# Kernel optimization log

Measured on AMD Instinct MI355X. Metric: run time of the kernel, lower is better.

## Reference

```python
import jax, jax.numpy as jnp
import numpy as np

N, E, M, NT, RB, SH, NIR, LAT = 10000, 160000, 8, 4, 8, 9, 3, 128
AVG_N = 16.0
LATF = LAT + M * NIR  # 152
COMP2IR = np.array([0, 1, 1, 1, 2, 2, 2, 2, 2])  # irrep id per SH component (0e,1o,2e)
IR1H = jnp.asarray(np.eye(NIR, dtype=np.float32)[COMP2IR])  # [9,3] one-hot comp->irrep


def _silu(x):
    return x * jax.nn.sigmoid(x)


def setup_inputs() -> dict:
    key = jax.random.key(0)
    ks = jax.random.split(key, 16)
    def w(k, shape, fan_in):
        return jax.random.normal(k, shape, jnp.float32) / np.sqrt(fan_in)
    return {
        'edge_attrs': jax.random.normal(ks[0], (E, SH), jnp.float32),
        'edge_embedding': jax.random.normal(ks[1], (E, RB), jnp.float32),
        'node_attrs': jax.random.uniform(ks[2], (N, NT), jnp.float32),
        'edge_lengths': jax.random.uniform(ks[3], (E,), jnp.float32),
        'tb_w0': w(ks[4], (2 * NT + RB, LAT), 2 * NT + RB),
        'tb_w1': w(ks[5], (LAT, LAT), LAT),
        'tb_w2': w(ks[6], (LAT, LAT), LAT),
        'env_mlp_w0': w(ks[7], (LAT, 2 * M * NIR), LAT),
        'env_mlp_w1': w(ks[8], (LAT, M * NIR), LAT),
        'env_linear_w': w(ks[9], (2, NIR, M, M), M),
        'latent_w': w(ks[10], (LATF, LAT), LATF),
        'lat2feat_w': w(ks[11], (2, LATF, NIR * M * M), LATF),
        'lat2featold_w': w(ks[12], (2, LATF, NIR * M * M), LATF),
        'final_w': w(ks[13], (LATF, M), LATF),
        'edge_index': jax.random.randint(ks[14], (2, E), 0, N, jnp.int32),
    }


def reference(edge_attrs, edge_embedding, node_attrs, edge_lengths,
              tb_w0, tb_w1, tb_w2, env_mlp_w0, env_mlp_w1, env_linear_w,
              latent_w, lat2feat_w, lat2featold_w, final_w, edge_index):
    center, neigh = edge_index[0], edge_index[1]
    n_nodes = node_attrs.shape[0]
    c2i = jnp.asarray(COMP2IR)

    # polynomial cutoff, p=6, x = r / r_max
    x = edge_lengths
    p = 6.0
    cut = (1.0 - (p + 1) * (p + 2) / 2 * x**6 + p * (p + 2) * x**7 - p * (p + 1) / 2 * x**8)
    cut = jnp.where(x < 1.0, cut, 0.0)[:, None]

    # two-body latent MLP on [center species, neighbor species, radial basis]
    tb_in = jnp.concatenate([node_attrs[center], node_attrs[neigh], edge_embedding], axis=-1)
    h = _silu(tb_in @ tb_w0)
    h = _silu(h @ tb_w1)
    latents = (h @ tb_w2) * cut  # [E, LAT]

    def weight_edges(wch):  # MakeWeightedChannels: per-irrep channel weights
        return wch[:, :, c2i] * edge_attrs[:, None, :]  # [E, M, 9]

    def env_of(w_cur, layer):  # scatter to node env + env linear
        env = jax.ops.segment_sum(weight_edges(w_cur), center, num_segments=n_nodes) / AVG_N
        Wc = env_linear_w[layer][c2i]  # [9, M, M]
        return jnp.einsum('duv,nvd->nud', Wc, env) / np.sqrt(M)

    def interact(features, env_c):  # scalar-gated equivariant coupling
        return features * env_c[:, :, :1] + env_c * features[:, :, :1]

    def invariants(f):  # per-(channel, irrep) norms
        return jnp.sqrt(jnp.einsum('eud,di->eui', f * f, IR1H) + 1e-8).reshape(f.shape[0], M * NIR)

    def pe_linear(Wflat, f):  # per-edge generated irrep-wise Linear
        W = Wflat.reshape(-1, NIR, M, M)
        return jnp.einsum('eiuv,di,evd->eud', W, IR1H, f) / np.sqrt(M)

    # ---- layer 0 (initial weighter + env weighter) ----
    ew = latents @ env_mlp_w0  # [E, 2*M*NIR]
    w_init = ew[:, :M * NIR].reshape(-1, M, NIR)
    w_cur = ew[:, M * NIR:].reshape(-1, M, NIR)
    features = weight_edges(w_init)  # [E, M, 9]
    env_c = env_of(w_cur, 0)[center]
    new_f = interact(features, env_c)
    lat_full = jnp.concatenate([latents, invariants(new_f)], axis=-1)  # [E, 152]
    features = 0.5 * pe_linear(lat_full @ lat2featold_w[0], features) \
             + 0.5 * pe_linear(lat_full @ lat2feat_w[0], new_f)

    # ---- layer 1 ----
    lat_new = _silu(lat_full @ latent_w) * cut
    latents = 0.5 * latents + 0.5 * lat_new  # latent resnet, sigmoid(0)=0.5
    w_cur = (latents @ env_mlp_w1).reshape(-1, M, NIR)
    env_c = env_of(w_cur, 1)[center]
    new_f = interact(features, env_c)
    lat_full = jnp.concatenate([latents, invariants(new_f)], axis=-1)
    features = 0.5 * pe_linear(lat_full @ lat2featold_w[1], features) \
             + 0.5 * pe_linear(lat_full @ lat2feat_w[1], new_f)

    # ---- final: generated linear to 1x1o per edge (components 1:4) ----
    wfin = lat_full @ final_w  # [E, M]
    return jnp.einsum('em,emd->ed', wfin, features[:, :, 1:4]) / np.sqrt(M)
```

## Files before the change

### kernel.cpp

```cpp
#include <hip/hip_runtime.h>
#include <hip/hip_bf16.h>

#define EE 160000
#define NNODES 10000

using bf16 = __hip_bfloat16;
using bf16x8 = __attribute__((ext_vector_type(8))) short;
using short4v = __attribute__((ext_vector_type(4))) short;
using f32x4  = __attribute__((ext_vector_type(4))) float;

__device__ __forceinline__ float silu_f(float x) { return x / (1.0f + __expf(-x)); }
__device__ __forceinline__ float b2f(bf16 v) { return __bfloat162float(v); }
__device__ __forceinline__ bf16 f2b(float v) { return __float2bfloat16(v); }

__device__ __forceinline__ unsigned bfbits(float v) {
    union { float f; unsigned u; } a; a.f = v;
    return (a.u + 0x7fffu + ((a.u >> 16) & 1u)) >> 16;
}
__device__ __forceinline__ unsigned pack2(float a, float b) {
    return bfbits(a) | (bfbits(b) << 16);
}
__device__ __forceinline__ void unpack2(unsigned u, float& a, float& b) {
    union { unsigned x; float f; } lo, hi;
    lo.x = u << 16; hi.x = u & 0xffff0000u;
    a = lo.f; b = hi.f;
}
__device__ __forceinline__ float bs2f(short s) {
    union { unsigned u; float f; } x; x.u = ((unsigned)(unsigned short)s) << 16;
    return x.f;
}

#define INV_AVGN_SQM 0.02209708691207961f
#define HALF_INV_SQM 0.17677669529663687f
#define INV_SQM      0.35355339059327373f

__global__ void kCnt(const int* __restrict__ eidx, int* __restrict__ deg)
{
    const int e = blockIdx.x * 256 + threadIdx.x;
    atomicAdd(&deg[eidx[e]], 1);
}

__global__ void kScan(const int* __restrict__ deg, int* __restrict__ off)
{
    __shared__ int part[256];
    const int t = threadIdx.x;
    int loc[40];
    int s = 0;
#pragma unroll
    for (int i = 0; i < 40; i++) {
        const int idx = t * 40 + i;
        const int v = (idx < NNODES) ? deg[idx] : 0;
        loc[i] = s;
        s += v;
    }
    part[t] = s;
    __syncthreads();
    for (int d = 1; d < 256; d <<= 1) {
        const int v = (t >= d) ? part[t - d] : 0;
        __syncthreads();
        part[t] += v;
        __syncthreads();
    }
    const int base = (t == 0) ? 0 : part[t - 1];
#pragma unroll
    for (int i = 0; i < 40; i++) {
        const int idx = t * 40 + i;
        if (idx < NNODES) off[idx] = base + loc[i];
    }
    if (t == 255) off[NNODES] = part[255];
}

__global__ void kFill(const int* __restrict__ eidx, int* __restrict__ cur,
                      const int* __restrict__ off, int* __restrict__ elist)
{
    const int e = blockIdx.x * 256 + threadIdx.x;
    const int c = eidx[e];
    const int pos = atomicAdd(&cur[c], 1);
    elist[off[c] + pos] = e;
}

__global__ void kPrepA(const float* __restrict__ w1, const float* __restrict__ w2,
                       const float* __restrict__ wm0, short* __restrict__ wAtF)
{
    const int t = blockIdx.x * 256 + threadIdx.x;
    if (t >= 38912) return;
    const int k = t & 127, c = t >> 7;
    float v;
    if (c < 128)      v = w1[k * 128 + c];
    else if (c < 256) v = w2[k * 128 + (c - 128)];
    else              v = wm0[k * 48 + (c - 256)];
    wAtF[((k >> 3) * 304 + c) * 8 + (k & 7)] = (short)bfbits(v);
}

__global__ void kPrepB(const float* __restrict__ l2fo, const float* __restrict__ l2fn,
                       const float* __restrict__ latw, const float* __restrict__ l2fo1,
                       const float* __restrict__ l2fn1, const float* __restrict__ finw,
                       const float* __restrict__ wm1, short* __restrict__ BtF)
{
    const int k = blockIdx.y;
    const int col = blockIdx.x * 256 + threadIdx.x;
    if (col >= 672) return;
    float v = 0.f;
    if (col < 648) {
        if (k < 152) {
            if (col < 384) {
                const int ir = col >> 7, half = (col >> 6) & 1, q = col & 63;
                const float* src = half ? l2fn : l2fo;
                v = src[k * 192 + ir * 64 + q];
            } else if (col < 512)  v = latw[k * 128 + (col - 384)];
            else if (col < 576)    v = l2fo1[k * 192 + 64 + (col - 512)];
            else if (col < 640)    v = l2fn1[k * 192 + 64 + (col - 576)];
            else                   v = finw[k * 8 + (col - 640)];
        }
    } else {
        if (k < 128) v = wm1[k * 24 + (col - 648)];
    }
    BtF[((k >> 3) * 672 + col) * 8 + (k & 7)] = (short)bfbits(v);
}

__global__ void kEnvG(const float* __restrict__ wcur, const float* __restrict__ ea,
                      const int* __restrict__ off, const int* __restrict__ elist,
                      const float* __restrict__ wl, float* __restrict__ envc)
{
    const int t = blockIdx.x * 256 + threadIdx.x;
    if (t >= NNODES * 9) return;
    const int n = t / 9;
    const int d = t - n * 9;
    const int irr = (d == 0) ? 0 : ((d < 4) ? 1 : 2);
    float v[8];
#pragma unroll
    for (int q = 0; q < 8; q++) v[q] = 0.0f;
    const int b = off[n], en = off[n + 1];
    for (int j = b; j < en; j++) {
        const int e = elist[j];
        const float ad = ea[e * 9 + d];
        const float* wr = wcur + (size_t)e * 24 + irr;
#pragma unroll
        for (int q = 0; q < 8; q++) v[q] = fmaf(wr[q * 3], ad, v[q]);
    }
#pragma unroll
    for (int u = 0; u < 8; u++) {
        float s = 0.0f;
#pragma unroll
        for (int q = 0; q < 8; q++) s = fmaf(wl[irr * 64 + u * 8 + q], v[q], s);
        envc[n * 72 + u * 9 + d] = s * INV_AVGN_SQM;
    }
}

__global__ __launch_bounds__(256) void kA0(
    const float* __restrict__ ea, const float* __restrict__ eemb,
    const float* __restrict__ nat, const float* __restrict__ elen,
    const float* __restrict__ w0, const int* __restrict__ eidx,
    short* __restrict__ h08, short* __restrict__ latf8s,
    bf16* __restrict__ eaT, float* __restrict__ cutb)
{
    __shared__ float w0s[16 * 128];
    const int t = threadIdx.x;
    const int e = blockIdx.x * 256 + t;
#pragma unroll
    for (int p = 0; p < 8; p++) { const int idx = p * 256 + t; w0s[idx] = w0[idx]; }
    __syncthreads();

    const int ctr = eidx[e];
    const int ngb = eidx[EE + e];
    float tin[16];
#pragma unroll
    for (int k = 0; k < 4; k++) tin[k] = nat[ctr * 4 + k];
#pragma unroll
    for (int k = 0; k < 4; k++) tin[4 + k] = nat[ngb * 4 + k];
#pragma unroll
    for (int k = 0; k < 8; k++) tin[8 + k] = eemb[e * 8 + k];

    const float x = elen[e];
    const float x2 = x * x, x4 = x2 * x2, x6 = x4 * x2, x7 = x6 * x, x8 = x7 * x;
    float cutv = 1.0f - 28.0f * x6 + 48.0f * x7 - 21.0f * x8;
    cutv = (x < 1.0f) ? cutv : 0.0f;
    cutb[e] = cutv;

    const size_t tb = (size_t)(e >> 5);
    const int el = e & 31;
#pragma unroll
    for (int jc = 0; jc < 4; jc++) {
        float a[32];
#pragma unroll
        for (int j = 0; j < 32; j++) a[j] = 0.0f;
#pragma unroll
        for (int k = 0; k < 16; k++) {
            const float v = tin[k];
#pragma unroll
            for (int j = 0; j < 32; j++) a[j] = fmaf(v, w0s[k * 128 + jc * 32 + j], a[j]);
        }
#pragma unroll
        for (int cc = 0; cc < 4; cc++) {
            bf16x8 hv;
#pragma unroll
            for (int jj = 0; jj < 8; jj++) hv[jj] = (short)bfbits(silu_f(a[cc * 8 + jj]));
            *(bf16x8*)(h08 + tb * 4096 + (jc * 4 + cc) * 256 + el * 8) = hv;
        }
    }
    bf16x8 z;
#pragma unroll
    for (int jj = 0; jj < 8; jj++) z[jj] = 0;
    *(bf16x8*)(latf8s + tb * 5120 + 19 * 256 + el * 8) = z;

#pragma unroll
    for (int d = 0; d < 9; d++) eaT[(size_t)d * EE + e] = f2b(ea[e * 9 + d]);
}

__global__ __launch_bounds__(256, 4) void kAm(
    const short* __restrict__ h08, const short* __restrict__ wAtF,
    const float* __restrict__ cutb, short* __restrict__ latf8s,
    float* __restrict__ winiF, float* __restrict__ wcur0)
{
    __shared__ alignas(16) char a2raw[16384];
    __shared__ short A3[8192];
    short* A2 = (short*)a2raw;
    float* Cs = (float*)a2raw;

    const int t = threadIdx.x;
    const int eb = blockIdx.x * 64;
    const int lane = t & 63, wid = t >> 6;
    const int wm = wid >> 1, wn = wid & 1;
    const int l15 = lane & 15, kq = lane >> 4;
    const f32x4 zz = {0.f, 0.f, 0.f, 0.f};

    float cutR[2][4];
#pragma unroll
    for (int mi = 0; mi < 2; mi++)
#pragma unroll
        for (int r = 0; r < 4; r++)
            cutR[mi][r] = cutb[eb + wm * 32 + mi * 16 + kq * 4 + r];

    {
        f32x4 acc[8];
#pragma unroll
        for (int q = 0; q < 8; q++) acc[q] = zz;
        const size_t ab = (size_t)((eb >> 5) + wm) * 4096 + l15 * 8;
#pragma unroll
        for (int ks = 0; ks < 4; ks++) {
            const int kc = ks * 4 + kq;
            const bf16x8 a0 = *(const bf16x8*)(h08 + ab + kc * 256);
            const bf16x8 a1 = *(const bf16x8*)(h08 + ab + kc * 256 + 128);
            const short* bp = wAtF + (kc * 304 + wn * 64 + l15) * 8;
#pragma unroll
            for (int ni = 0; ni < 4; ni++) {
                const bf16x8 b = *(const bf16x8*)(bp + ni * 16 * 8);
                acc[ni]     = __builtin_amdgcn_mfma_f32_16x16x32_bf16(a0, b, acc[ni], 0, 0, 0);
                acc[4 + ni] = __builtin_amdgcn_mfma_f32_16x16x32_bf16(a1, b, acc[4 + ni], 0, 0, 0);
            }
        }
#pragma unroll
        for (int mi = 0; mi < 2; mi++)
#pragma unroll
            for (int ni = 0; ni < 4; ni++) {
                const int kcol = wn * 64 + ni * 16 + l15;
                const int eb2 = wm * 32 + mi * 16 + (kq << 2);
#pragma unroll
                for (int r = 0; r < 4; r++)
                    A2[(kcol >> 3) * 512 + (eb2 + r) * 8 + (kcol & 7)] =
                        (short)bfbits(silu_f(acc[mi * 4 + ni][r]));
            }
    }
    __syncthreads();

    {
        f32x4 acc[8];
#pragma unroll
        for (int q = 0; q < 8; q++) acc[q] = zz;
#pragma unroll
        for (int ks = 0; ks < 4; ks++) {
            const int kc = ks * 4 + kq;
            const bf16x8 a0 = *(const bf16x8*)(A2 + kc * 512 + (wm * 32 + l15) * 8);
            const bf16x8 a1 = *(const bf16x8*)(A2 + kc * 512 + (wm * 32 + 16 + l15) * 8);
            const short* bp = wAtF + (kc * 304 + 128 + wn * 64 + l15) * 8;
#pragma unroll
            for (int ni = 0; ni < 4; ni++) {
                const bf16x8 b = *(const bf16x8*)(bp + ni * 16 * 8);
                acc[ni]     = __builtin_amdgcn_mfma_f32_16x16x32_bf16(a0, b, acc[ni], 0, 0, 0);
                acc[4 + ni] = __builtin_amdgcn_mfma_f32_16x16x32_bf16(a1, b, acc[4 + ni], 0, 0, 0);
            }
        }
#pragma unroll
        for (int mi = 0; mi < 2; mi++)
#pragma unroll
            for (int ni = 0; ni < 4; ni++) {
                const int kcol = wn * 64 + ni * 16 + l15;
                const int eb2 = wm * 32 + mi * 16 + (kq << 2);
#pragma unroll
                for (int r = 0; r < 4; r++)
                    A3[(kcol >> 3) * 512 + (eb2 + r) * 8 + (kcol & 7)] =
                        (short)bfbits(acc[mi * 4 + ni][r] * cutR[mi][r]);
            }
    }
    __syncthreads();
#pragma unroll
    for (int p = 0; p < 4; p++) {
        const int i = p * 256 + t;
        const int e = i & 63, kc = i >> 6;
        const bf16x8 v = *(const bf16x8*)(A3 + kc * 512 + e * 8);
        const int eg = eb + e;
        *(bf16x8*)(latf8s + (size_t)(eg >> 5) * 5120 + kc * 256 + (eg & 31) * 8) = v;
    }

    if (wn == 0) {
        f32x4 acc[6];
#pragma unroll
        for (int q = 0; q < 6; q++) acc[q] = zz;
#pragma unroll
        for (int ks = 0; ks < 4; ks++) {
            const int kc = ks * 4 + kq;
            const bf16x8 a0 = *(const bf16x8*)(A3 + kc * 512 + (wm * 32 + l15) * 8);
            const bf16x8 a1 = *(const bf16x8*)(A3 + kc * 512 + (wm * 32 + 16 + l15) * 8);
            const short* bp = wAtF + (kc * 304 + 256 + l15) * 8;
#pragma unroll
            for (int ni = 0; ni < 3; ni++) {
                const bf16x8 b = *(const bf16x8*)(bp + ni * 16 * 8);
                acc[ni]     = __builtin_amdgcn_mfma_f32_16x16x32_bf16(a0, b, acc[ni], 0, 0, 0);
                acc[3 + ni] = __builtin_amdgcn_mfma_f32_16x16x32_bf16(a1, b, acc[3 + ni], 0, 0, 0);
            }
        }
#pragma unroll
        for (int mi = 0; mi < 2; mi++)
#pragma unroll
            for (int ni = 0; ni < 3; ni++) {
                const int c = ni * 16 + l15;
                const int eb2 = wm * 32 + mi * 16 + (kq << 2);
#pragma unroll
                for (int r = 0; r < 4; r++)
                    Cs[c * 65 + eb2 + r] = acc[mi * 3 + ni][r];
            }
    }
    __syncthreads();
    for (int i = t; i < 1536; i += 256) {
        const int c = i >> 6, e = i & 63;
        winiF[(size_t)c * EE + eb + e] = Cs[c * 65 + e];
    }
    for (int i = t; i < 1536; i += 256) {
        const int e2 = i / 24, c2 = i - e2 * 24;
        wcur0[(size_t)(eb + e2) * 24 + c2] = Cs[(24 + c2) * 65 + e2];
    }
}

__global__ __launch_bounds__(256, 1) void kC1(
    const float* __restrict__ winiF, const bf16* __restrict__ eaT,
    const float* __restrict__ envc, const int* __restrict__ eidx,
    unsigned* __restrict__ newfT, short* __restrict__ latf8s)
{
    const int e = blockIdx.x * 256 + threadIdx.x;
    const int ctr = eidx[e];
    float eav[9];
#pragma unroll
    for (int d = 0; d < 9; d++) eav[d] = b2f(eaT[(size_t)d * EE + e]);
    const float* ec = envc + ctr * 72;
    float inv[24];
#pragma unroll
    for (int uh = 0; uh < 4; uh++) {
        const int u0 = 2 * uh;
        float wi0[3], wi1[3];
#pragma unroll
        for (int i = 0; i < 3; i++) {
            wi0[i] = winiF[(size_t)(u0 * 3 + i) * EE + e];
            wi1[i] = winiF[(size_t)((u0 + 1) * 3 + i) * EE + e];
        }
        float nf0[9], nf1[9];
        const float ec00 = ec[u0 * 9 + 0];
        const float ec10 = ec[(u0 + 1) * 9 + 0];
        const float f00 = wi0[0] * eav[0];
        const float f10 = wi1[0] * eav[0];
#pragma unroll
        for (int d = 0; d < 9; d++) {
            const int irr = (d == 0) ? 0 : ((d < 4) ? 1 : 2);
            const float fa = wi0[irr] * eav[d];
            const float fb = wi1[irr] * eav[d];
            nf0[d] = fa * ec00 + ec[u0 * 9 + d] * f00;
            nf1[d] = fb * ec10 + ec[(u0 + 1) * 9 + d] * f10;
        }
#pragma unroll
        for (int d = 0; d < 9; d++) newfT[(size_t)(d * 4 + uh) * EE + e] = pack2(nf0[d], nf1[d]);
        inv[uh * 6 + 0] = sqrtf(nf0[0] * nf0[0] + 1e-8f);
        inv[uh * 6 + 1] = sqrtf(nf0[1]*nf0[1] + nf0[2]*nf0[2] + nf0[3]*nf0[3] + 1e-8f);
        inv[uh * 6 + 2] = sqrtf(nf0[4]*nf0[4] + nf0[5]*nf0[5] + nf0[6]*nf0[6] + nf0[7]*nf0[7] + nf0[8]*nf0[8] + 1e-8f);
        inv[uh * 6 + 3] = sqrtf(nf1[0] * nf1[0] + 1e-8f);
        inv[uh * 6 + 4] = sqrtf(nf1[1]*nf1[1] + nf1[2]*nf1[2] + nf1[3]*nf1[3] + 1e-8f);
        inv[uh * 6 + 5] = sqrtf(nf1[4]*nf1[4] + nf1[5]*nf1[5] + nf1[6]*nf1[6] + nf1[7]*nf1[7] + nf1[8]*nf1[8] + 1e-8f);
    }
    const size_t tb = (size_t)(e >> 5);
    const int el = e & 31;
#pragma unroll
    for (int j = 0; j < 3; j++) {
        bf16x8 iv;
#pragma unroll
        for (int jj = 0; jj < 8; jj++) iv[jj] = (short)bfbits(inv[j * 8 + jj]);
        *(bf16x8*)(latf8s + tb * 5120 + (16 + j) * 256 + el * 8) = iv;
    }
}

__global__ __launch_bounds__(256, 4) void kF0(
    const short* __restrict__ A8, const short* __restrict__ BtF,
    const float* __restrict__ winiF, const bf16* __restrict__ eaT,
    const unsigned* __restrict__ newfT, unsigned* __restrict__ feat1T)
{
    __shared__ float Cs[128 * 67];
    const int t = threadIdx.x;
    const int eb = blockIdx.x * 64;
    const int ir = blockIdx.y;
    const int lane = t & 63, wid = t >> 6;
    const int wm = wid >> 1, wn = wid & 1;
    const int l15 = lane & 15, kq = lane >> 4;
    const f32x4 zz = {0.f, 0.f, 0.f, 0.f};
    const size_t ab = (size_t)((eb >> 5) + wm) * 5120 + l15 * 8;
    const int te = t & 63, uh = t >> 6;
    const int eg = eb + te;

    f32x4 acc[8];
#pragma unroll
    for (int q = 0; q < 8; q++) acc[q] = zz;
#pragma unroll
    for (int ks = 0; ks < 5; ks++) {
        const int kc = ks * 4 + kq;
        const bf16x8 a0 = *(const bf16x8*)(A8 + ab + kc * 256);
        const bf16x8 a1 = *(const bf16x8*)(A8 + ab + kc * 256 + 128);
        const short* bp = BtF + (kc * 672 + ir * 128 + wn * 64 + l15) * 8;
#pragma unroll
        for (int ni = 0; ni < 4; ni++) {
            const bf16x8 b = *(const bf16x8*)(bp + ni * 16 * 8);
            acc[ni]     = __builtin_amdgcn_mfma_f32_16x16x32_bf16(a0, b, acc[ni], 0, 0, 0);
            acc[4 + ni] = __builtin_amdgcn_mfma_f32_16x16x32_bf16(a1, b, acc[4 + ni], 0, 0, 0);
        }
    }
#pragma unroll
    for (int mi = 0; mi < 2; mi++)
#pragma unroll
        for (int ni = 0; ni < 4; ni++) {
            const int cl = wn * 64 + ni * 16 + l15;
            const int el = wm * 32 + mi * 16 + (kq << 2);
            const f32x4 v = acc[mi * 4 + ni];
#pragma unroll
            for (int r = 0; r < 4; r++) Cs[cl * 67 + el + r] = v[r];
        }
    __syncthreads();
    const int d0 = (ir == 0) ? 0 : ((ir == 1) ? 1 : 4);
    const int nd = (ir == 0) ? 1 : ((ir == 1) ? 3 : 5);
    float wv[8];
#pragma unroll
    for (int v8 = 0; v8 < 8; v8++) wv[v8] = winiF[(size_t)(v8 * 3 + ir) * EE + eg];
    for (int dd = 0; dd < nd; dd++) {
        const int d = d0 + dd;
        const float ead = b2f(eaT[(size_t)d * EE + eg]);
        float nfv[8];
#pragma unroll
        for (int q = 0; q < 4; q++)
            unpack2(newfT[(size_t)(d * 4 + q) * EE + eg], nfv[2 * q], nfv[2 * q + 1]);
        float s0 = 0.f, s1 = 0.f;
#pragma unroll
        for (int v8 = 0; v8 < 8; v8++) {
            const float fe = wv[v8] * ead;
            s0 += Cs[(uh * 16 + v8) * 67 + te] * fe + Cs[(64 + uh * 16 + v8) * 67 + te] * nfv[v8];
            s1 += Cs[(uh * 16 + 8 + v8) * 67 + te] * fe + Cs[(64 + uh * 16 + 8 + v8) * 67 + te] * nfv[v8];
        }
        feat1T[(size_t)(d * 4 + uh) * EE + eg] = pack2(s0 * HALF_INV_SQM, s1 * HALF_INV_SQM);
    }
}

__global__ __launch_bounds__(256, 4) void kF3(
    short* __restrict__ A8, const short* __restrict__ BtF,
    const float* __restrict__ cutb, float* __restrict__ wcur1)
{
    __shared__ alignas(16) short Cc[128 * 68];
    __shared__ short l1s[16 * 512];
    float* Cw = (float*)Cc;
    const int t = threadIdx.x;
    const int eb = blockIdx.x * 64;
    const int lane = t & 63, wid = t >> 6;
    const int wm = wid >> 1, wn = wid & 1;
    const int l15 = lane & 15, kq = lane >> 4;
    const f32x4 zz = {0.f, 0.f, 0.f, 0.f};

    {
        f32x4 acc[8];
#pragma unroll
        for (int q = 0; q < 8; q++) acc[q] = zz;
        const size_t ab = (size_t)((eb >> 5) + wm) * 5120 + l15 * 8;
#pragma unroll
        for (int ks = 0; ks < 5; ks++) {
            const int kc = ks * 4 + kq;
            const bf16x8 a0 = *(const bf16x8*)(A8 + ab + kc * 256);
            const bf16x8 a1 = *(const bf16x8*)(A8 + ab + kc * 256 + 128);
            const short* bp = BtF + (kc * 672 + 384 + wn * 64 + l15) * 8;
#pragma unroll
            for (int ni = 0; ni < 4; ni++) {
                const bf16x8 b = *(const bf16x8*)(bp + ni * 16 * 8);
                acc[ni]     = __builtin_amdgcn_mfma_f32_16x16x32_bf16(a0, b, acc[ni], 0, 0, 0);
                acc[4 + ni] = __builtin_amdgcn_mfma_f32_16x16x32_bf16(a1, b, acc[4 + ni], 0, 0, 0);
            }
        }
#pragma unroll
        for (int mi = 0; mi < 2; mi++)
#pragma unroll
            for (int ni = 0; ni < 4; ni++) {
                const int cl = wn * 64 + ni * 16 + l15;
                const int el = wm * 32 + mi * 16 + (kq << 2);
                const f32x4 v = acc[mi * 4 + ni];
                short4v pv;
#pragma unroll
                for (int r = 0; r < 4; r++) pv[r] = (short)bfbits(v[r]);
                *(short4v*)(Cc + cl * 68 + el) = pv;
            }
    }
    __syncthreads();
    {
        const int te = t & 63, q = t >> 6;
        const int eg = eb + te;
        const size_t tb = (size_t)(eg >> 5);
        const int el2 = eg & 31;
        const float cutv = cutb[eg];
#pragma unroll
        for (int c = 0; c < 4; c++) {
            const int kc = q * 4 + c;
            short* ap = A8 + tb * 5120 + kc * 256 + el2 * 8;
            const bf16x8 ov = *(const bf16x8*)ap;
            bf16x8 nv;
#pragma unroll
            for (int jj = 0; jj < 8; jj++) {
                const int j = kc * 8 + jj;
                const float g = bs2f(Cc[j * 68 + te]);
                const float o = bs2f(ov[jj]);
                nv[jj] = (short)bfbits(0.5f * o + 0.5f * silu_f(g) * cutv);
            }
            *(bf16x8*)ap = nv;
            *(bf16x8*)(l1s + kc * 512 + te * 8) = nv;
        }
    }
    __syncthreads();
    if (wn == 0) {
        f32x4 acc[4] = {zz, zz, zz, zz};
#pragma unroll
        for (int ks = 0; ks < 4; ks++) {
            const int kc = ks * 4 + kq;
            const bf16x8 a0 = *(const bf16x8*)(l1s + kc * 512 + (wm * 32 + l15) * 8);
            const bf16x8 a1 = *(const bf16x8*)(l1s + kc * 512 + (wm * 32 + 16 + l15) * 8);
#pragma unroll
            for (int ni = 0; ni < 2; ni++) {
                const int c = ni * 16 + l15;
                bf16x8 b;
                if (c < 24) b = *(const bf16x8*)(BtF + (kc * 672 + 648 + c) * 8);
                else {
#pragma unroll
                    for (int jj = 0; jj < 8; jj++) b[jj] = 0;
                }
                acc[ni]     = __builtin_amdgcn_mfma_f32_16x16x32_bf16(a0, b, acc[ni], 0, 0, 0);
                acc[2 + ni] = __builtin_amdgcn_mfma_f32_16x16x32_bf16(a1, b, acc[2 + ni], 0, 0, 0);
            }
        }
#pragma unroll
        for (int mi = 0; mi < 2; mi++)
#pragma unroll
            for (int ni = 0; ni < 2; ni++) {
                const int c = ni * 16 + l15;
                if (c < 24) {
                    const int el = wm * 32 + mi * 16 + (kq << 2);
#pragma unroll
                    for (int r = 0; r < 4; r++) Cw[c * 65 + el + r] = acc[mi * 2 + ni][r];
                }
            }
    }
    __syncthreads();
    for (int i = t; i < 1536; i += 256) {
        const int e2 = i / 24, c2 = i - e2 * 24;
        wcur1[(size_t)(eb + e2) * 24 + c2] = Cw[c2 * 65 + e2];
    }
}

__global__ __launch_bounds__(256, 1) void kE1(
    const unsigned* __restrict__ feat1T, const float* __restrict__ envc,
    const int* __restrict__ eidx, unsigned* __restrict__ newfT,
    short* __restrict__ latf8s)
{
    const int e = blockIdx.x * 256 + threadIdx.x;
    const int ctr = eidx[e];
    const float* ec = envc + ctr * 72;
    float inv[24];
#pragma unroll
    for (int uh = 0; uh < 4; uh++) {
        const int u0 = 2 * uh;
        float f0[9], f1[9];
#pragma unroll
        for (int d = 0; d < 9; d++) unpack2(feat1T[(size_t)(d * 4 + uh) * EE + e], f0[d], f1[d]);
        const float ec00 = ec[u0 * 9 + 0];
        const float ec10 = ec[(u0 + 1) * 9 + 0];
        float nf0[9], nf1[9];
#pragma unroll
        for (int d = 0; d < 9; d++) {
            nf0[d] = f0[d] * ec00 + ec[u0 * 9 + d] * f0[0];
            nf1[d] = f1[d] * ec10 + ec[(u0 + 1) * 9 + d] * f1[0];
        }
#pragma unroll
        for (int d = 0; d < 9; d++) newfT[(size_t)(d * 4 + uh) * EE + e] = pack2(nf0[d], nf1[d]);
        inv[uh * 6 + 0] = sqrtf(nf0[0] * nf0[0] + 1e-8f);
        inv[uh * 6 + 1] = sqrtf(nf0[1]*nf0[1] + nf0[2]*nf0[2] + nf0[3]*nf0[3] + 1e-8f);
        inv[uh * 6 + 2] = sqrtf(nf0[4]*nf0[4] + nf0[5]*nf0[5] + nf0[6]*nf0[6] + nf0[7]*nf0[7] + nf0[8]*nf0[8] + 1e-8f);
        inv[uh * 6 + 3] = sqrtf(nf1[0] * nf1[0] + 1e-8f);
        inv[uh * 6 + 4] = sqrtf(nf1[1]*nf1[1] + nf1[2]*nf1[2] + nf1[3]*nf1[3] + 1e-8f);
        inv[uh * 6 + 5] = sqrtf(nf1[4]*nf1[4] + nf1[5]*nf1[5] + nf1[6]*nf1[6] + nf1[7]*nf1[7] + nf1[8]*nf1[8] + 1e-8f);
    }
    const size_t tb = (size_t)(e >> 5);
    const int el = e & 31;
#pragma unroll
    for (int j = 0; j < 3; j++) {
        bf16x8 iv;
#pragma unroll
        for (int jj = 0; jj < 8; jj++) iv[jj] = (short)bfbits(inv[j * 8 + jj]);
        *(bf16x8*)(latf8s + tb * 5120 + (16 + j) * 256 + el * 8) = iv;
    }
}

__global__ __launch_bounds__(256, 4) void kF2(
    const short* __restrict__ A8, const short* __restrict__ BtF,
    const unsigned* __restrict__ feat1T, const unsigned* __restrict__ newfT,
    float* __restrict__ outp)
{
    __shared__ float Cs[128 * 67];
    __shared__ float Cwf[16 * 67];
    const int t = threadIdx.x;
    const int eb = blockIdx.x * 64;
    const int lane = t & 63, wid = t >> 6;
    const int wm = wid >> 1, wn = wid & 1;
    const int l15 = lane & 15, kq = lane >> 4;
    const f32x4 zz = {0.f, 0.f, 0.f, 0.f};
    const size_t ab = (size_t)((eb >> 5) + wm) * 5120 + l15 * 8;

    {
        f32x4 acc[8];
#pragma unroll
        for (int q = 0; q < 8; q++) acc[q] = zz;
#pragma unroll
        for (int ks = 0; ks < 5; ks++) {
            const int kc = ks * 4 + kq;
            const bf16x8 a0 = *(const bf16x8*)(A8 + ab + kc * 256);
            const bf16x8 a1 = *(const bf16x8*)(A8 + ab + kc * 256 + 128);
            const short* bp = BtF + (kc * 672 + 512 + wn * 64 + l15) * 8;
#pragma unroll
            for (int ni = 0; ni < 4; ni++) {
                const bf16x8 b = *(const bf16x8*)(bp + ni * 16 * 8);
                acc[ni]     = __builtin_amdgcn_mfma_f32_16x16x32_bf16(a0, b, acc[ni], 0, 0, 0);
                acc[4 + ni] = __builtin_amdgcn_mfma_f32_16x16x32_bf16(a1, b, acc[4 + ni], 0, 0, 0);
            }
        }
#pragma unroll
        for (int mi = 0; mi < 2; mi++)
#pragma unroll
            for (int ni = 0; ni < 4; ni++) {
                const int cl = wn * 64 + ni * 16 + l15;
                const int el = wm * 32 + mi * 16 + (kq << 2);
                const f32x4 v = acc[mi * 4 + ni];
#pragma unroll
                for (int r = 0; r < 4; r++) Cs[cl * 67 + el + r] = v[r];
            }
    }
    {
        f32x4 a2[2] = {zz, zz};
        bf16x8 bz;
#pragma unroll
        for (int jj = 0; jj < 8; jj++) bz[jj] = 0;
#pragma unroll
        for (int ks = 0; ks < 5; ks++) {
            const int kc = ks * 4 + kq;
            const bf16x8 a0 = *(const bf16x8*)(A8 + ab + kc * 256);
            const bf16x8 a1 = *(const bf16x8*)(A8 + ab + kc * 256 + 128);
            const bf16x8 b = (l15 < 8)
                ? *(const bf16x8*)(BtF + (kc * 672 + 640 + l15) * 8) : bz;
            a2[0] = __builtin_amdgcn_mfma_f32_16x16x32_bf16(a0, b, a2[0], 0, 0, 0);
            a2[1] = __builtin_amdgcn_mfma_f32_16x16x32_bf16(a1, b, a2[1], 0, 0, 0);
        }
        if (wn == 0) {
#pragma unroll
            for (int mi = 0; mi < 2; mi++) {
                const int el = wm * 32 + mi * 16 + (kq << 2);
#pragma unroll
                for (int r = 0; r < 4; r++) Cwf[l15 * 67 + el + r] = a2[mi][r];
            }
        }
    }
    __syncthreads();
    if (t < 192) {
        const int te = t % 64;
        const int dd = t / 64;
        const int eg = eb + te;
        const int d = 1 + dd;
        float f1v[8], nfv[8];
#pragma unroll
        for (int q = 0; q < 4; q++) {
            unpack2(feat1T[(size_t)(d * 4 + q) * EE + eg], f1v[2 * q], f1v[2 * q + 1]);
            unpack2(newfT[(size_t)(d * 4 + q) * EE + eg], nfv[2 * q], nfv[2 * q + 1]);
        }
        float od = 0.f;
#pragma unroll
        for (int u = 0; u < 8; u++) {
            float s = 0.f;
#pragma unroll
            for (int v8 = 0; v8 < 8; v8++)
                s += Cs[(u * 8 + v8) * 67 + te] * f1v[v8] + Cs[(64 + u * 8 + v8) * 67 + te] * nfv[v8];
            od = fmaf(Cwf[u * 67 + te], s, od);
        }
        outp[(size_t)eg * 3 + dd] = od * (HALF_INV_SQM * INV_SQM);
    }
}

extern "C" void kernel_launch(void* const* d_in, const int* in_sizes, int n_in,
                              void* d_out, int out_size, void* d_ws, size_t ws_size,
                              hipStream_t stream)
{
    const float* ea   = (const float*)d_in[0];
    const float* eemb = (const float*)d_in[1];
    const float* nat  = (const float*)d_in[2];
    const float* elen = (const float*)d_in[3];
    const float* w0   = (const float*)d_in[4];
    const float* w1   = (const float*)d_in[5];
    const float* w2   = (const float*)d_in[6];
    const float* wm0  = (const float*)d_in[7];
    const float* wm1  = (const float*)d_in[8];
    const float* envl = (const float*)d_in[9];
    const float* latw = (const float*)d_in[10];
    const float* l2fn = (const float*)d_in[11];
    const float* l2fo = (const float*)d_in[12];
    const float* finw = (const float*)d_in[13];
    const int*   eidx = (const int*)d_in[14];

    char* ws = (char*)d_ws;
    short*    latf8s = (short*)(ws + 0);
    short*    h08    = (short*)(ws + 51200000);
    unsigned* newfT  = (unsigned*)(ws + 92160000);
    unsigned* feat1T = (unsigned*)(ws + 115200000);
    float*    winiF  = (float*)(ws + 138240000);
    bf16*     eaT    = (bf16*)(ws + 153600000);
    float*    cutb   = (float*)(ws + 156480000);
    float*    env0   = (float*)(ws + 157120000);
    float*    env1   = (float*)(ws + 160000000);
    int*      deg    = (int*)(ws + 162880000);
    int*      cur    = (int*)(ws + 162920000);
    int*      off    = (int*)(ws + 162960000);
    int*      elist  = (int*)(ws + 163000192);
    short*    wAtF   = (short*)(ws + 162880000);
    short*    BtF    = (short*)(ws + 163640192);

    float* wcur0 = (float*)newfT;
    float* wcur1 = (float*)newfT;

    hipMemsetAsync(deg, 0, 80000, stream);

    kCnt <<<625, 256, 0, stream>>>(eidx, deg);
    kScan<<<1, 256, 0, stream>>>(deg, off);
    kFill<<<625, 256, 0, stream>>>(eidx, cur, off, elist);
    kPrepA<<<152, 256, 0, stream>>>(w1, w2, wm0, wAtF);
    kPrepB<<<dim3(3, 160), 256, 0, stream>>>(l2fo, l2fn, latw,
                                             l2fo + 29184, l2fn + 29184, finw, wm1, BtF);

    kA0<<<625, 256, 0, stream>>>(ea, eemb, nat, elen, w0, eidx, h08, latf8s, eaT, cutb);
    kAm<<<2500, 256, 0, stream>>>(h08, wAtF, cutb, latf8s, winiF, wcur0);
    kEnvG<<<352, 256, 0, stream>>>(wcur0, ea, off, elist, envl + 0, env0);
    kC1<<<625, 256, 0, stream>>>(winiF, eaT, env0, eidx, newfT, latf8s);

    kF0<<<dim3(2500, 3), 256, 0, stream>>>(latf8s, BtF, winiF, eaT, newfT, feat1T);
    kF3<<<2500, 256, 0, stream>>>(latf8s, BtF, cutb, wcur1);
    kEnvG<<<352, 256, 0, stream>>>(wcur1, ea, off, elist, envl + 192, env1);
    kE1<<<625, 256, 0, stream>>>(feat1T, env1, eidx, newfT, latf8s);
    kF2<<<2500, 256, 0, stream>>>(latf8s, BtF, feat1T, newfT, (float*)d_out);
}
```

Baseline: 290.5 us.

## Shrink LDS staging to bf16, raise occupancy, fuse final-weight GEMM into kF2

The kF0 and kF2 epilogues now round MFMA outputs to bf16 and stage them in shared memory as packed shorts with stride 68, halving LDS use, and launch bounds are raised to allow more resident blocks. kF3 drops its l1s shared buffer and re-reads the updated latents from global memory. kF2 merges the separate final_w GEMM pass into the main loop on the wn==1 waves, so the A operand is loaded once. The trade-off is extra bf16 rounding of intermediate weights, global re-reads that rely on cache hits, and tighter register budgets that could cause spills.

```diff
diff --git a/kernel.cpp b/kernel.cpp
--- a/kernel.cpp
+++ b/kernel.cpp
@@ -395,12 +395,12 @@
     }
 }
 
-__global__ __launch_bounds__(256, 4) void kF0(
+__global__ __launch_bounds__(256, 8) void kF0(
     const short* __restrict__ A8, const short* __restrict__ BtF,
     const float* __restrict__ winiF, const bf16* __restrict__ eaT,
     const unsigned* __restrict__ newfT, unsigned* __restrict__ feat1T)
 {
-    __shared__ float Cs[128 * 67];
+    __shared__ alignas(16) short Cs[128 * 68];
     const int t = threadIdx.x;
     const int eb = blockIdx.x * 64;
     const int ir = blockIdx.y;
@@ -435,8 +435,10 @@
             const int cl = wn * 64 + ni * 16 + l15;
             const int el = wm * 32 + mi * 16 + (kq << 2);
             const f32x4 v = acc[mi * 4 + ni];
-#pragma unroll
-            for (int r = 0; r < 4; r++) Cs[cl * 67 + el + r] = v[r];
+            short4v pv;
+#pragma unroll
+            for (int r = 0; r < 4; r++) pv[r] = (short)bfbits(v[r]);
+            *(short4v*)(Cs + cl * 68 + el) = pv;
         }
     __syncthreads();
     const int d0 = (ir == 0) ? 0 : ((ir == 1) ? 1 : 4);
@@ -455,19 +457,18 @@
 #pragma unroll
         for (int v8 = 0; v8 < 8; v8++) {
             const float fe = wv[v8] * ead;
-            s0 += Cs[(uh * 16 + v8) * 67 + te] * fe + Cs[(64 + uh * 16 + v8) * 67 + te] * nfv[v8];
-            s1 += Cs[(uh * 16 + 8 + v8) * 67 + te] * fe + Cs[(64 + uh * 16 + 8 + v8) * 67 + te] * nfv[v8];
+            s0 += bs2f(Cs[(uh * 16 + v8) * 68 + te]) * fe + bs2f(Cs[(64 + uh * 16 + v8) * 68 + te]) * nfv[v8];
+            s1 += bs2f(Cs[(uh * 16 + 8 + v8) * 68 + te]) * fe + bs2f(Cs[(64 + uh * 16 + 8 + v8) * 68 + te]) * nfv[v8];
         }
         feat1T[(size_t)(d * 4 + uh) * EE + eg] = pack2(s0 * HALF_INV_SQM, s1 * HALF_INV_SQM);
     }
 }
 
-__global__ __launch_bounds__(256, 4) void kF3(
+__global__ __launch_bounds__(256, 6) void kF3(
     short* __restrict__ A8, const short* __restrict__ BtF,
     const float* __restrict__ cutb, float* __restrict__ wcur1)
 {
     __shared__ alignas(16) short Cc[128 * 68];
-    __shared__ short l1s[16 * 512];
     float* Cw = (float*)Cc;
     const int t = threadIdx.x;
     const int eb = blockIdx.x * 64;
@@ -475,12 +476,12 @@
     const int wm = wid >> 1, wn = wid & 1;
     const int l15 = lane & 15, kq = lane >> 4;
     const f32x4 zz = {0.f, 0.f, 0.f, 0.f};
+    const size_t ab = (size_t)((eb >> 5) + wm) * 5120 + l15 * 8;
 
     {
         f32x4 acc[8];
 #pragma unroll
         for (int q = 0; q < 8; q++) acc[q] = zz;
-        const size_t ab = (size_t)((eb >> 5) + wm) * 5120 + l15 * 8;
 #pragma unroll
         for (int ks = 0; ks < 5; ks++) {
             const int kc = ks * 4 + kq;
@@ -528,7 +529,6 @@
                 nv[jj] = (short)bfbits(0.5f * o + 0.5f * silu_f(g) * cutv);
             }
             *(bf16x8*)ap = nv;
-            *(bf16x8*)(l1s + kc * 512 + te * 8) = nv;
         }
     }
     __syncthreads();
@@ -537,8 +537,8 @@
 #pragma unroll
         for (int ks = 0; ks < 4; ks++) {
             const int kc = ks * 4 + kq;
-            const bf16x8 a0 = *(const bf16x8*)(l1s + kc * 512 + (wm * 32 + l15) * 8);
-            const bf16x8 a1 = *(const bf16x8*)(l1s + kc * 512 + (wm * 32 + 16 + l15) * 8);
+            const bf16x8 a0 = *(const bf16x8*)(A8 + ab + kc * 256);
+            const bf16x8 a1 = *(const bf16x8*)(A8 + ab + kc * 256 + 128);
 #pragma unroll
             for (int ni = 0; ni < 2; ni++) {
                 const int c = ni * 16 + l15;
@@ -614,13 +614,13 @@
     }
 }
 
-__global__ __launch_bounds__(256, 4) void kF2(
+__global__ __launch_bounds__(256, 6) void kF2(
     const short* __restrict__ A8, const short* __restrict__ BtF,
     const unsigned* __restrict__ feat1T, const unsigned* __restrict__ newfT,
     float* __restrict__ outp)
 {
-    __shared__ float Cs[128 * 67];
-    __shared__ float Cwf[16 * 67];
+    __shared__ alignas(16) short Cs[128 * 68];
+    __shared__ alignas(16) short Cwf[16 * 68];
     const int t = threadIdx.x;
     const int eb = blockIdx.x * 64;
     const int lane = t & 63, wid = t >> 6;
@@ -630,9 +630,12 @@
     const size_t ab = (size_t)((eb >> 5) + wm) * 5120 + l15 * 8;
 
     {
-        f32x4 acc[8];
-#pragma unroll
-        for (int q = 0; q < 8; q++) acc[q] = zz;
+        f32x4 acc[10];
+#pragma unroll
+        for (int q = 0; q < 10; q++) acc[q] = zz;
+        bf16x8 bz;
+#pragma unroll
+        for (int jj = 0; jj < 8; jj++) bz[jj] = 0;
 #pragma unroll
         for (int ks = 0; ks < 5; ks++) {
             const int kc = ks * 4 + kq;
@@ -645,6 +648,12 @@
                 acc[ni]     = __builtin_amdgcn_mfma_f32_16x16x32_bf16(a0, b, acc[ni], 0, 0, 0);
                 acc[4 + ni] = __builtin_amdgcn_mfma_f32_16x16x32_bf16(a1, b, acc[4 + ni], 0, 0, 0);
             }
+            if (wn == 1) {
+                const bf16x8 b5 = (l15 < 8)
+                    ? *(const bf16x8*)(BtF + (kc * 672 + 640 + l15) * 8) : bz;
+                acc[8] = __builtin_amdgcn_mfma_f32_16x16x32_bf16(a0, b5, acc[8], 0, 0, 0);
+                acc[9] = __builtin_amdgcn_mfma_f32_16x16x32_bf16(a1, b5, acc[9], 0, 0, 0);
+            }
         }
 #pragma unroll
         for (int mi = 0; mi < 2; mi++)
@@ -653,31 +662,20 @@
                 const int cl = wn * 64 + ni * 16 + l15;
                 const int el = wm * 32 + mi * 16 + (kq << 2);
                 const f32x4 v = acc[mi * 4 + ni];
-#pragma unroll
-                for (int r = 0; r < 4; r++) Cs[cl * 67 + el + r] = v[r];
-            }
-    }
-    {
-        f32x4 a2[2] = {zz, zz};
-        bf16x8 bz;
-#pragma unroll
-        for (int jj = 0; jj < 8; jj++) bz[jj] = 0;
-#pragma unroll
-        for (int ks = 0; ks < 5; ks++) {
-            const int kc = ks * 4 + kq;
-            const bf16x8 a0 = *(const bf16x8*)(A8 + ab + kc * 256);
-            const bf16x8 a1 = *(const bf16x8*)(A8 + ab + kc * 256 + 128);
-            const bf16x8 b = (l15 < 8)
-                ? *(const bf16x8*)(BtF + (kc * 672 + 640 + l15) * 8) : bz;
-            a2[0] = __builtin_amdgcn_mfma_f32_16x16x32_bf16(a0, b, a2[0], 0, 0, 0);
-            a2[1] = __builtin_amdgcn_mfma_f32_16x16x32_bf16(a1, b, a2[1], 0, 0, 0);
-        }
-        if (wn == 0) {
+                short4v pv;
+#pragma unroll
+                for (int r = 0; r < 4; r++) pv[r] = (short)bfbits(v[r]);
+                *(short4v*)(Cs + cl * 68 + el) = pv;
+            }
+        if (wn == 1) {
 #pragma unroll
             for (int mi = 0; mi < 2; mi++) {
                 const int el = wm * 32 + mi * 16 + (kq << 2);
-#pragma unroll
-                for (int r = 0; r < 4; r++) Cwf[l15 * 67 + el + r] = a2[mi][r];
+                const f32x4 v = acc[8 + mi];
+                short4v pv;
+#pragma unroll
+                for (int r = 0; r < 4; r++) pv[r] = (short)bfbits(v[r]);
+                *(short4v*)(Cwf + l15 * 68 + el) = pv;
             }
         }
     }
@@ -699,8 +697,8 @@
             float s = 0.f;
 #pragma unroll
             for (int v8 = 0; v8 < 8; v8++)
-                s += Cs[(u * 8 + v8) * 67 + te] * f1v[v8] + Cs[(64 + u * 8 + v8) * 67 + te] * nfv[v8];
-            od = fmaf(Cwf[u * 67 + te], s, od);
+                s += bs2f(Cs[(u * 8 + v8) * 68 + te]) * f1v[v8] + bs2f(Cs[(64 + u * 8 + v8) * 68 + te]) * nfv[v8];
+            od = fmaf(bs2f(Cwf[u * 68 + te]), s, od);
         }
         outp[(size_t)eg * 3 + dd] = od * (HALF_INV_SQM * INV_SQM);
     }
```

After: 295.5 us. About the same (+1.7%).
